# Performance work log

Measured on AMD Instinct MI355X. Metric: run time of the kernel, lower is better.

## Reference

```python
import jax, jax.numpy as jnp
import numpy as np

B, N, COUT, CIN, H, W = 16, 4, 256, 256, 64, 64


def setup_inputs() -> dict:
    key = jax.random.key(0)
    k1, k2, k3, k4 = jax.random.split(key, 4)
    x = jax.random.normal(k1, (B, CIN, H, W), jnp.float32)
    alphas = jax.random.uniform(k2, (B, N), jnp.float32)          # routing weights (lambdas)
    angles = jax.random.normal(k3, (B, N), jnp.float32) * 0.5     # thetas, mixed signs
    # kaiming_normal_(mode='fan_out', relu): std = sqrt(2 / (Cout * k * k))
    std = np.sqrt(2.0 / (COUT * 9)).astype(np.float32)
    weight = jax.random.normal(k4, (N, COUT, CIN, 3, 3), jnp.float32) * std
    return {"x": x, "alphas": alphas, "angles": angles, "weight": weight}


def _rot_mats(thetas):
    """thetas: [M] -> rotation matrices [M, 9, 9] (row, col), matching torch builder."""
    xc = jnp.cos(thetas)
    ys = jnp.sin(thetas)
    a = xc - ys
    b = xc * ys
    c = xc + ys
    z = jnp.zeros_like(xc)
    o = jnp.ones_like(xc)

    def mat(rows):
        # rows: list of 9 lists of 9 [M]-arrays -> [M, 9, 9]
        return jnp.stack([jnp.stack(r, axis=-1) for r in rows], axis=-2)

    pos = mat([
        [a, 1 - a, z, z, z, z, z, z, z],
        [z, xc - b, b, z, 1 - c + b, ys - b, z, z, z],
        [z, z, a, z, z, 1 - a, z, z, z],
        [b, ys - b, z, xc - b, 1 - c + b, z, z, z, z],
        [z, z, z, z, o, z, z, z, z],
        [z, z, z, z, 1 - c + b, xc - b, z, ys - b, b],
        [z, z, z, 1 - a, z, z, a, z, z],
        [z, z, z, ys - b, 1 - c + b, z, b, xc - b, z],
        [z, z, z, z, z, z, z, 1 - a, a],
    ])
    neg = mat([
        [c, z, z, 1 - c, z, z, z, z, z],
        [-b, xc + b, z, b - ys, 1 - a - b, z, z, z, z],
        [z, 1 - c, c, z, z, z, z, z, z],
        [z, z, z, xc + b, 1 - a - b, z, -b, b - ys, z],
        [z, z, z, z, o, z, z, z, z],
        [z, b - ys, -b, z, 1 - a - b, xc + b, z, z, z],
        [z, z, z, z, z, z, c, 1 - c, z],
        [z, z, z, z, 1 - a - b, b - ys, z, xc + b, -b],
        [z, z, z, z, z, 1 - c, z, z, c],
    ])
    m = (thetas >= 0).astype(thetas.dtype)[:, None, None]
    return m * pos + (1 - m) * neg


def reference(x, alphas, angles, weight):
    bsz, Cin, h, w = x.shape
    n, Cout = weight.shape[0], weight.shape[1]
    # [bsz, n, 9, 9] rotation matrices scaled by routing lambdas
    rm = _rot_mats(angles.reshape(-1)).reshape(bsz, n, 9, 9)
    rm = rm * alphas[:, :, None, None]
    # weights [n, Cout, Cin, 3, 3] -> [n, 9, Cout*Cin]
    Wf = weight.transpose(0, 3, 4, 1, 2).reshape(n, 9, Cout * Cin)
    # mix over kernel_number n and source tap q -> per-sample rotated kernels
    rw = jnp.einsum('bnpq,nqm->bpm', rm, Wf)          # [bsz, 9, Cout*Cin]
    rw = rw.reshape(bsz, 3, 3, Cout, Cin).transpose(0, 3, 4, 1, 2)
    rw = rw.reshape(bsz * Cout, Cin, 3, 3)
    # per-sample conv via grouped conv on flattened batch
    xr = x.reshape(1, bsz * Cin, h, w)
    out = jax.lax.conv_general_dilated(
        xr, rw, window_strides=(1, 1), padding=((1, 1), (1, 1)),
        dimension_numbers=('NCHW', 'OIHW', 'NCHW'), feature_group_count=bsz)
    return out.reshape(bsz, Cout, out.shape[2], out.shape[3])
```

## Files before the change

kernel.cpp:

```cpp
#include <hip/hip_runtime.h>
#include <hip/hip_bf16.h>

#define B_    16
#define N_    4
#define COUT  256
#define CIN   256
#define H_    64
#define W_    64
#define K_TOT (CIN * 9)
#define HW    (H_ * W_)
#define NKT   36
#define PAD   66
#define PLANE (PAD * PAD)

typedef __attribute__((ext_vector_type(8))) short short8;
typedef __attribute__((ext_vector_type(4))) float f32x4;
typedef unsigned short ushort_t;

static __device__ __forceinline__ ushort_t f2bf(float f) {
    __hip_bfloat16 h = __float2bfloat16(f);
    return *reinterpret_cast<ushort_t*>(&h);
}

typedef __attribute__((address_space(3))) unsigned int lds_u32;
typedef __attribute__((address_space(1))) const unsigned int glb_u32;
static __device__ __forceinline__ void gl_lds16(const ushort_t* g, ushort_t* l) {
    __builtin_amdgcn_global_load_lds((glb_u32*)g, (lds_u32*)l, 16, 0, 0);
}

#define BARRIER() asm volatile("s_barrier" ::: "memory")
#define VMCNTN(N) asm volatile("s_waitcnt vmcnt(" #N ")" ::: "memory")

__global__ __launch_bounds__(256)
void build_rw_kernel(const float* __restrict__ weight,
                     const float* __restrict__ alphas,
                     const float* __restrict__ angles,
                     ushort_t* __restrict__ rw) {
    __shared__ float rms[N_ * 81];
    int tid = threadIdx.x;
    int b = blockIdx.y;

    if (tid < N_) {
        int i = b * N_ + tid;
        float th = angles[i], al = alphas[i];
        float xc = cosf(th), ys = sinf(th);
        float a = xc - ys, bb = xc * ys, c = xc + ys;
        float r[81];
#pragma unroll
        for (int j = 0; j < 81; ++j) r[j] = 0.f;
        if (th >= 0.f) {
            r[0] = a;          r[1] = 1.f - a;
            r[10] = xc - bb;   r[11] = bb;       r[13] = 1.f - c + bb; r[14] = ys - bb;
            r[20] = a;         r[23] = 1.f - a;
            r[27] = bb;        r[28] = ys - bb;  r[30] = xc - bb;      r[31] = 1.f - c + bb;
            r[40] = 1.f;
            r[49] = 1.f - c + bb; r[50] = xc - bb; r[52] = ys - bb;    r[53] = bb;
            r[57] = 1.f - a;   r[60] = a;
            r[66] = ys - bb;   r[67] = 1.f - c + bb; r[69] = bb;       r[70] = xc - bb;
            r[79] = 1.f - a;   r[80] = a;
        } else {
            r[0] = c;          r[3] = 1.f - c;
            r[9] = -bb;        r[10] = xc + bb;  r[12] = bb - ys;      r[13] = 1.f - a - bb;
            r[19] = 1.f - c;   r[20] = c;
            r[30] = xc + bb;   r[31] = 1.f - a - bb; r[33] = -bb;      r[34] = bb - ys;
            r[40] = 1.f;
            r[46] = bb - ys;   r[47] = -bb;      r[49] = 1.f - a - bb; r[50] = xc + bb;
            r[60] = c;         r[61] = 1.f - c;
            r[67] = 1.f - a - bb; r[68] = bb - ys; r[70] = xc + bb;    r[71] = -bb;
            r[77] = 1.f - c;   r[80] = c;
        }
#pragma unroll
        for (int j = 0; j < 81; ++j) rms[tid * 81 + j] = r[j] * al;
    }
    __syncthreads();

    int idx = blockIdx.x * 256 + tid;
    int cout = idx >> 8, cin = idx & 255;

    float wv[N_][9];
#pragma unroll
    for (int n = 0; n < N_; ++n)
#pragma unroll
        for (int q = 0; q < 9; ++q)
            wv[n][q] = weight[(size_t)(n * (COUT * CIN) + idx) * 9 + q];

    ushort_t* dst = rw + (size_t)(b * COUT + cout) * K_TOT + cin;
#pragma unroll
    for (int p = 0; p < 9; ++p) {
        float s = 0.f;
#pragma unroll
        for (int n = 0; n < N_; ++n)
#pragma unroll
            for (int q = 0; q < 9; ++q)
                s += rms[n * 81 + p * 9 + q] * wv[n][q];
        dst[p * 256] = f2bf(s);
    }
}

__global__ __launch_bounds__(256)
void nhwc_kernel(const float* __restrict__ x, ushort_t* __restrict__ xt) {
    int y    = blockIdx.x;
    int cb32 = blockIdx.y;
    int b    = blockIdx.z;
    __shared__ ushort_t tileT[64][40];
    int t = threadIdx.x;

    ushort_t* plane = xt + (size_t)(b * 4 + (cb32 >> 1)) * PLANE * 64 + (cb32 & 1) * 32;
    const int4 z = {0, 0, 0, 0};

    int ci = t & 31, seg = t >> 5;
    const float* src = x + ((size_t)(b * CIN + cb32 * 32 + ci) * HW + y * 64 + seg * 8);
    float4 f0 = ((const float4*)src)[0];
    float4 f1 = ((const float4*)src)[1];
#pragma unroll
    for (int q = 0; q < 4; ++q) tileT[seg * 8 + q][ci]     = f2bf(((float*)&f0)[q]);
#pragma unroll
    for (int q = 0; q < 4; ++q) tileT[seg * 8 + 4 + q][ci] = f2bf(((float*)&f1)[q]);

    if (t < 8) {
        int col = (t >> 2) ? 65 : 0;
        int sg  = t & 3;
        *(int4*)(plane + ((size_t)(y + 1) * PAD + col) * 64 + sg * 8) = z;
    }
    if (y == 0) {
        for (int u = t; u < 528; u += 256) {
            int row = (u >= 264) ? 65 : 0;
            int v = (u >= 264) ? u - 264 : u;
            int px = v >> 2, sg = v & 3;
            *(int4*)(plane + ((size_t)row * PAD + px) * 64 + sg * 8) = z;
        }
    }
    __syncthreads();

    int px = t >> 2, cseg = t & 3;
    ushort_t* dst = plane + ((size_t)(y + 1) * PAD + px + 1) * 64 + cseg * 8;
    *(int4*)dst = *(const int4*)&tileT[px][cseg * 8];
}

__global__ __launch_bounds__(512, 1)
void conv_kernel(const ushort_t* __restrict__ xt,
                 const ushort_t* __restrict__ rw,
                 float* __restrict__ out) {
    int bid0 = blockIdx.x;
    int bid = (bid0 & 7) * 32 + (bid0 >> 3);
    int b     = bid >> 4;
    int ptile = bid & 15;
    int y0 = ptile * 4;
    int tid = threadIdx.x;
    int lane = tid & 63, wid = tid >> 6;
    int wm = wid >> 2, wn = wid & 3;
    int rA = lane & 15, kseg = lane >> 4;

    __shared__ __align__(16) ushort_t As[2][16384];
    __shared__ __align__(16) ushort_t Bs[2][16384];
    ushort_t* AsB = &As[0][0];
    ushort_t* BsB = &Bs[0][0];

    f32x4 acc[8][4] = {};

    const ushort_t* rwb = rw + (size_t)b * COUT * K_TOT;
    const ushort_t* xtb = xt + ((size_t)b * 4 * PLANE + (size_t)y0 * PAD) * 64;

    const int rq = tid >> 3;
    const int cs = ((tid & 7) ^ (rq & 7)) * 8;
    const int dl = tid * 8;

#define RSLOT(KH) ((((KH) << 2) | kseg) ^ (rA & 7)) * 8

#define STAGE_A2(KT, Q, Q0, Q1)                                                \
    {                                                                          \
        int p_ = (KT) >> 2, c4_ = (KT) & 3;                                    \
        int ako = p_ * 256 + c4_ * 64;                                         \
        gl_lds16(rwb + (size_t)((Q0) * 64 + rq) * K_TOT + cs + ako,            \
                 AsB + (Q) * 16384 + (Q0) * 4096 + dl);                        \
        gl_lds16(rwb + (size_t)((Q1) * 64 + rq) * K_TOT + cs + ako,            \
                 AsB + (Q) * 16384 + (Q1) * 4096 + dl);                        \
    }

#define STAGE_B2(KT, Q, Q0, Q1)                                                \
    {                                                                          \
        int p_ = (KT) >> 2, c4_ = (KT) & 3;                                    \
        int ph_ = p_ / 3, pw_ = p_ - 3 * ph_;                                  \
        const ushort_t* sb_ = xtb + (size_t)(c4_ * PLANE + ph_ * PAD + pw_) * 64; \
        gl_lds16(sb_ + (size_t)((Q0) * PAD + rq) * 64 + cs,                    \
                 BsB + (Q) * 16384 + (Q0) * 4096 + dl);                        \
        gl_lds16(sb_ + (size_t)((Q1) * PAD + rq) * 64 + cs,                    \
                 BsB + (Q) * 16384 + (Q1) * 4096 + dl);                        \
    }

#define READ_AF(Q, MH, KH)                                                     \
    _Pragma("unroll")                                                          \
    for (int mi = 0; mi < 4; ++mi) {                                           \
        int row = wm * 128 + (MH) * 64 + mi * 16 + rA;                         \
        af[mi] = *(const short8*)(AsB + (Q) * 16384 + row * 64 + RSLOT(KH));   \
    }

#define READ_BF(Q, KH)                                                         \
    _Pragma("unroll")                                                          \
    for (int ni = 0; ni < 4; ++ni) {                                           \
        int row = wn * 64 + ni * 16 + rA;                                      \
        bf[ni] = *(const short8*)(BsB + (Q) * 16384 + row * 64 + RSLOT(KH));   \
    }

#define DO_MFMA(MH)                                                            \
    __builtin_amdgcn_s_setprio(1);                                             \
    _Pragma("unroll")                                                          \
    for (int mi = 0; mi < 4; ++mi)                                             \
        _Pragma("unroll")                                                      \
        for (int ni = 0; ni < 4; ++ni)                                         \
            acc[(MH) * 4 + mi][ni] = __builtin_amdgcn_mfma_f32_16x16x32_bf16(  \
                af[mi], bf[ni], acc[(MH) * 4 + mi][ni], 0, 0, 0);              \
    __builtin_amdgcn_s_setprio(0);

    STAGE_B2(0, 0, 0, 1);
    STAGE_B2(0, 0, 2, 3);
    STAGE_A2(0, 0, 0, 2);
    STAGE_A2(0, 0, 1, 3);
    VMCNTN(2);
    BARRIER();

    short8 af[4], bf[4];
    for (int kt = 0; kt < NKT; ++kt) {
        int q = kt & 1, qn = q ^ 1;
        bool more = (kt + 1 < NKT);
        READ_AF(q, 0, 0);
        READ_BF(q, 0);
        if (more) STAGE_B2(kt + 1, qn, 0, 1);
        BARRIER();
        DO_MFMA(0);
        if (more) { VMCNTN(2); } else { VMCNTN(0); }
        BARRIER();
        READ_AF(q, 1, 0);
        if (more) STAGE_B2(kt + 1, qn, 2, 3);
        BARRIER();
        DO_MFMA(1);
        BARRIER();
        READ_AF(q, 0, 1);
        READ_BF(q, 1);
        if (more) STAGE_A2(kt + 1, qn, 0, 2);
        BARRIER();
        DO_MFMA(0);
        BARRIER();
        READ_AF(q, 1, 1);
        if (more) STAGE_A2(kt + 1, qn, 1, 3);
        BARRIER();
        DO_MFMA(1);
        VMCNTN(2);
        BARRIER();
    }
#undef STAGE_A2
#undef STAGE_B2
#undef READ_AF
#undef READ_BF
#undef DO_MFMA
#undef RSLOT

    int row0 = (lane >> 4) * 4;
    int col  = lane & 15;
    float* outb = out + (size_t)b * COUT * HW + ptile * 256;
#pragma unroll
    for (int am = 0; am < 8; ++am)
#pragma unroll
        for (int an = 0; an < 4; ++an)
#pragma unroll
            for (int rr = 0; rr < 4; ++rr) {
                int m = wm * 128 + am * 16 + row0 + rr;
                int n = wn * 64 + an * 16 + col;
                outb[(size_t)m * HW + n] = acc[am][an][rr];
            }
}

extern "C" void kernel_launch(void* const* d_in, const int* in_sizes, int n_in,
                              void* d_out, int out_size, void* d_ws, size_t ws_size,
                              hipStream_t stream) {
    const float* x      = (const float*)d_in[0];
    const float* alphas = (const float*)d_in[1];
    const float* angles = (const float*)d_in[2];
    const float* weight = (const float*)d_in[3];
    float* out = (float*)d_out;

    ushort_t* rw = (ushort_t*)d_ws;
    ushort_t* xt = (ushort_t*)((char*)d_ws + (size_t)B_ * COUT * K_TOT * 2);

    build_rw_kernel<<<dim3(COUT * CIN / 256, B_), 256, 0, stream>>>(weight, alphas, angles, rw);
    nhwc_kernel<<<dim3(64, 8, B_), 256, 0, stream>>>(x, xt);
    conv_kernel<<<256, 512, 0, stream>>>(xt, rw, out);
}
```

Measured before the change: 107.5 us.

## Triple-buffer the activation tile to prefetch two K-steps ahead

The B (activation) LDS buffer grows from two stages to three, so B tiles are loaded two iterations ahead while A weights stay double-buffered one step ahead. The staging order inside each iteration is reshuffled so A loads are issued first and B loads later, and the vmcnt waits are retuned to allow more outstanding global-to-LDS loads. The aim is to hide more global-load latency behind the MFMA work. The cost is 32 KB more LDS (160 KB total), which leaves less headroom and makes the wait-count bookkeeping more fragile.

```diff
diff --git a/kernel.cpp b/kernel.cpp
--- a/kernel.cpp
+++ b/kernel.cpp
@@ -152,7 +152,7 @@
     int rA = lane & 15, kseg = lane >> 4;
 
     __shared__ __align__(16) ushort_t As[2][16384];
-    __shared__ __align__(16) ushort_t Bs[2][16384];
+    __shared__ __align__(16) ushort_t Bs[3][16384];
     ushort_t* AsB = &As[0][0];
     ushort_t* BsB = &Bs[0][0];
 
@@ -167,39 +167,39 @@
 
 #define RSLOT(KH) ((((KH) << 2) | kseg) ^ (rA & 7)) * 8
 
-#define STAGE_A2(KT, Q, Q0, Q1)                                                \
+#define STAGE_A2(KT, BUFO, Q0, Q1)                                             \
     {                                                                          \
         int p_ = (KT) >> 2, c4_ = (KT) & 3;                                    \
         int ako = p_ * 256 + c4_ * 64;                                         \
         gl_lds16(rwb + (size_t)((Q0) * 64 + rq) * K_TOT + cs + ako,            \
-                 AsB + (Q) * 16384 + (Q0) * 4096 + dl);                        \
+                 AsB + (BUFO) + (Q0) * 4096 + dl);                             \
         gl_lds16(rwb + (size_t)((Q1) * 64 + rq) * K_TOT + cs + ako,            \
-                 AsB + (Q) * 16384 + (Q1) * 4096 + dl);                        \
-    }
-
-#define STAGE_B2(KT, Q, Q0, Q1)                                                \
+                 AsB + (BUFO) + (Q1) * 4096 + dl);                             \
+    }
+
+#define STAGE_B2(KT, BUFO, Q0, Q1)                                             \
     {                                                                          \
         int p_ = (KT) >> 2, c4_ = (KT) & 3;                                    \
         int ph_ = p_ / 3, pw_ = p_ - 3 * ph_;                                  \
         const ushort_t* sb_ = xtb + (size_t)(c4_ * PLANE + ph_ * PAD + pw_) * 64; \
         gl_lds16(sb_ + (size_t)((Q0) * PAD + rq) * 64 + cs,                    \
-                 BsB + (Q) * 16384 + (Q0) * 4096 + dl);                        \
+                 BsB + (BUFO) + (Q0) * 4096 + dl);                             \
         gl_lds16(sb_ + (size_t)((Q1) * PAD + rq) * 64 + cs,                    \
-                 BsB + (Q) * 16384 + (Q1) * 4096 + dl);                        \
-    }
-
-#define READ_AF(Q, MH, KH)                                                     \
+                 BsB + (BUFO) + (Q1) * 4096 + dl);                             \
+    }
+
+#define READ_AF(BUFO, MH, KH)                                                  \
     _Pragma("unroll")                                                          \
     for (int mi = 0; mi < 4; ++mi) {                                           \
         int row = wm * 128 + (MH) * 64 + mi * 16 + rA;                         \
-        af[mi] = *(const short8*)(AsB + (Q) * 16384 + row * 64 + RSLOT(KH));   \
-    }
-
-#define READ_BF(Q, KH)                                                         \
+        af[mi] = *(const short8*)(AsB + (BUFO) + row * 64 + RSLOT(KH));        \
+    }
+
+#define READ_BF(BUFO, KH)                                                      \
     _Pragma("unroll")                                                          \
     for (int ni = 0; ni < 4; ++ni) {                                           \
         int row = wn * 64 + ni * 16 + rA;                                      \
-        bf[ni] = *(const short8*)(BsB + (Q) * 16384 + row * 64 + RSLOT(KH));   \
+        bf[ni] = *(const short8*)(BsB + (BUFO) + row * 64 + RSLOT(KH));        \
     }
 
 #define DO_MFMA(MH)                                                            \
@@ -216,37 +216,48 @@
     STAGE_B2(0, 0, 2, 3);
     STAGE_A2(0, 0, 0, 2);
     STAGE_A2(0, 0, 1, 3);
-    VMCNTN(2);
+    STAGE_B2(1, 16384, 0, 1);
+    STAGE_B2(1, 16384, 2, 3);
+    VMCNTN(6);
     BARRIER();
 
     short8 af[4], bf[4];
+    int bq = 0;
     for (int kt = 0; kt < NKT; ++kt) {
-        int q = kt & 1, qn = q ^ 1;
-        bool more = (kt + 1 < NKT);
-        READ_AF(q, 0, 0);
-        READ_BF(q, 0);
-        if (more) STAGE_B2(kt + 1, qn, 0, 1);
+        int bsq = bq + 2; if (bsq >= 3) bsq -= 3;
+        const int abuf  = (kt & 1) << 14;
+        const int anbuf = ((kt + 1) & 1) << 14;
+        const int bbuf  = bq * 16384;
+        const int bsbuf = bsq * 16384;
+        bool moreA = (kt + 1 < NKT), moreB = (kt + 2 < NKT);
+
+        READ_AF(abuf, 0, 0);
+        READ_BF(bbuf, 0);
+        if (moreA) STAGE_A2(kt + 1, anbuf, 0, 2);
         BARRIER();
         DO_MFMA(0);
-        if (more) { VMCNTN(2); } else { VMCNTN(0); }
-        BARRIER();
-        READ_AF(q, 1, 0);
-        if (more) STAGE_B2(kt + 1, qn, 2, 3);
+        if (moreA) { VMCNTN(6); } else { VMCNTN(0); }
+        BARRIER();
+        READ_AF(abuf, 1, 0);
+        if (moreA) STAGE_A2(kt + 1, anbuf, 1, 3);
         BARRIER();
         DO_MFMA(1);
         BARRIER();
-        READ_AF(q, 0, 1);
-        READ_BF(q, 1);
-        if (more) STAGE_A2(kt + 1, qn, 0, 2);
+        READ_AF(abuf, 0, 1);
+        READ_BF(bbuf, 1);
+        if (moreB) STAGE_B2(kt + 2, bsbuf, 0, 1);
         BARRIER();
         DO_MFMA(0);
         BARRIER();
-        READ_AF(q, 1, 1);
-        if (more) STAGE_A2(kt + 1, qn, 1, 3);
+        READ_AF(abuf, 1, 1);
+        if (moreB) STAGE_B2(kt + 2, bsbuf, 2, 3);
         BARRIER();
         DO_MFMA(1);
-        VMCNTN(2);
-        BARRIER();
+        if (moreB)      { VMCNTN(6); }
+        else if (moreA) { VMCNTN(2); }
+        else            { VMCNTN(0); }
+        BARRIER();
+        bq = (bq == 2) ? 0 : bq + 1;
     }
 #undef STAGE_A2
 #undef STAGE_B2
```

After: 107.2 us. Within noise of the previous version (-0.2%).

## Switch conv GEMM to 32x32x16 MFMA tiles with two-phase K pipeline

Applied to the files above, without the earlier changes.

Replaces the 16x16x32 bf16 MFMA tiling with 32x32x16 MFMAs, so each wave holds a 4x2 grid of 32x32 accumulators. The LDS fragment reads, the swizzled slot addressing and the output scatter are rewritten to match the new layout. The per-k-tile schedule shrinks from four barrier phases to two, staging half of the next tile's A and B loads in each phase. The aim is fewer LDS reads per MFMA and fewer barriers, at the cost of more register pressure from the larger fragment arrays.

```diff
diff --git a/kernel.cpp b/kernel.cpp
--- a/kernel.cpp
+++ b/kernel.cpp
@@ -14,7 +14,7 @@
 #define PLANE (PAD * PAD)
 
 typedef __attribute__((ext_vector_type(8))) short short8;
-typedef __attribute__((ext_vector_type(4))) float f32x4;
+typedef __attribute__((ext_vector_type(16))) float f32x16;
 typedef unsigned short ushort_t;
 
 static __device__ __forceinline__ ushort_t f2bf(float f) {
@@ -149,14 +149,15 @@
     int tid = threadIdx.x;
     int lane = tid & 63, wid = tid >> 6;
     int wm = wid >> 2, wn = wid & 3;
-    int rA = lane & 15, kseg = lane >> 4;
+    int rA = lane & 31;
+    int hi = lane >> 5;
 
     __shared__ __align__(16) ushort_t As[2][16384];
     __shared__ __align__(16) ushort_t Bs[2][16384];
     ushort_t* AsB = &As[0][0];
     ushort_t* BsB = &Bs[0][0];
 
-    f32x4 acc[8][4] = {};
+    f32x16 acc[4][2] = {};
 
     const ushort_t* rwb = rw + (size_t)b * COUT * K_TOT;
     const ushort_t* xtb = xt + ((size_t)b * 4 * PLANE + (size_t)y0 * PAD) * 64;
@@ -165,108 +166,104 @@
     const int cs = ((tid & 7) ^ (rq & 7)) * 8;
     const int dl = tid * 8;
 
-#define RSLOT(KH) ((((KH) << 2) | kseg) ^ (rA & 7)) * 8
-
-#define STAGE_A2(KT, Q, Q0, Q1)                                                \
+#define RSLOT(KS) ((((KS) * 2 + hi) ^ (lane & 7)) * 8)
+
+#define STAGE_A1(KT, BUFO, QTR)                                                \
     {                                                                          \
         int p_ = (KT) >> 2, c4_ = (KT) & 3;                                    \
         int ako = p_ * 256 + c4_ * 64;                                         \
-        gl_lds16(rwb + (size_t)((Q0) * 64 + rq) * K_TOT + cs + ako,            \
-                 AsB + (Q) * 16384 + (Q0) * 4096 + dl);                        \
-        gl_lds16(rwb + (size_t)((Q1) * 64 + rq) * K_TOT + cs + ako,            \
-                 AsB + (Q) * 16384 + (Q1) * 4096 + dl);                        \
-    }
-
-#define STAGE_B2(KT, Q, Q0, Q1)                                                \
+        gl_lds16(rwb + (size_t)((QTR) * 64 + rq) * K_TOT + cs + ako,           \
+                 AsB + (BUFO) + (QTR) * 4096 + dl);                            \
+    }
+
+#define STAGE_B1(KT, BUFO, QTR)                                                \
     {                                                                          \
         int p_ = (KT) >> 2, c4_ = (KT) & 3;                                    \
         int ph_ = p_ / 3, pw_ = p_ - 3 * ph_;                                  \
         const ushort_t* sb_ = xtb + (size_t)(c4_ * PLANE + ph_ * PAD + pw_) * 64; \
-        gl_lds16(sb_ + (size_t)((Q0) * PAD + rq) * 64 + cs,                    \
-                 BsB + (Q) * 16384 + (Q0) * 4096 + dl);                        \
-        gl_lds16(sb_ + (size_t)((Q1) * PAD + rq) * 64 + cs,                    \
-                 BsB + (Q) * 16384 + (Q1) * 4096 + dl);                        \
-    }
-
-#define READ_AF(Q, MH, KH)                                                     \
+        gl_lds16(sb_ + (size_t)((QTR) * PAD + rq) * 64 + cs,                   \
+                 BsB + (BUFO) + (QTR) * 4096 + dl);                            \
+    }
+
+#define READ_AF(BUFO, MH)                                                      \
     _Pragma("unroll")                                                          \
-    for (int mi = 0; mi < 4; ++mi) {                                           \
-        int row = wm * 128 + (MH) * 64 + mi * 16 + rA;                         \
-        af[mi] = *(const short8*)(AsB + (Q) * 16384 + row * 64 + RSLOT(KH));   \
-    }
-
-#define READ_BF(Q, KH)                                                         \
+    for (int mi = 0; mi < 2; ++mi) {                                           \
+        int row = wm * 128 + ((MH) * 2 + mi) * 32 + rA;                        \
+        _Pragma("unroll")                                                      \
+        for (int ks = 0; ks < 4; ++ks)                                         \
+            af[mi][ks] = *(const short8*)(AsB + (BUFO) + row * 64 + RSLOT(ks));\
+    }
+
+#define READ_BF(BUFO)                                                          \
     _Pragma("unroll")                                                          \
-    for (int ni = 0; ni < 4; ++ni) {                                           \
-        int row = wn * 64 + ni * 16 + rA;                                      \
-        bf[ni] = *(const short8*)(BsB + (Q) * 16384 + row * 64 + RSLOT(KH));   \
+    for (int ni = 0; ni < 2; ++ni) {                                           \
+        int row = wn * 64 + ni * 32 + rA;                                      \
+        _Pragma("unroll")                                                      \
+        for (int ks = 0; ks < 4; ++ks)                                         \
+            bf[ni][ks] = *(const short8*)(BsB + (BUFO) + row * 64 + RSLOT(ks));\
     }
 
 #define DO_MFMA(MH)                                                            \
     __builtin_amdgcn_s_setprio(1);                                             \
     _Pragma("unroll")                                                          \
-    for (int mi = 0; mi < 4; ++mi)                                             \
+    for (int mi = 0; mi < 2; ++mi)                                             \
         _Pragma("unroll")                                                      \
-        for (int ni = 0; ni < 4; ++ni)                                         \
-            acc[(MH) * 4 + mi][ni] = __builtin_amdgcn_mfma_f32_16x16x32_bf16(  \
-                af[mi], bf[ni], acc[(MH) * 4 + mi][ni], 0, 0, 0);              \
+        for (int ni = 0; ni < 2; ++ni)                                         \
+            _Pragma("unroll")                                                  \
+            for (int ks = 0; ks < 4; ++ks)                                     \
+                acc[(MH) * 2 + mi][ni] = __builtin_amdgcn_mfma_f32_32x32x16_bf16( \
+                    af[mi][ks], bf[ni][ks], acc[(MH) * 2 + mi][ni], 0, 0, 0);  \
     __builtin_amdgcn_s_setprio(0);
 
-    STAGE_B2(0, 0, 0, 1);
-    STAGE_B2(0, 0, 2, 3);
-    STAGE_A2(0, 0, 0, 2);
-    STAGE_A2(0, 0, 1, 3);
+    STAGE_A1(0, 0, 0); STAGE_A1(0, 0, 2);
+    STAGE_B1(0, 0, 0); STAGE_B1(0, 0, 1);
+    STAGE_B1(0, 0, 2); STAGE_B1(0, 0, 3);
+    STAGE_A1(0, 0, 1); STAGE_A1(0, 0, 3);
     VMCNTN(2);
     BARRIER();
 
-    short8 af[4], bf[4];
+    short8 af[2][4], bf[2][4];
     for (int kt = 0; kt < NKT; ++kt) {
-        int q = kt & 1, qn = q ^ 1;
+        const int qb  = (kt & 1) << 14;
+        const int qnb = ((kt + 1) & 1) << 14;
         bool more = (kt + 1 < NKT);
-        READ_AF(q, 0, 0);
-        READ_BF(q, 0);
-        if (more) STAGE_B2(kt + 1, qn, 0, 1);
+        READ_BF(qb);
+        READ_AF(qb, 0);
+        if (more) {
+            STAGE_A1(kt + 1, qnb, 0); STAGE_A1(kt + 1, qnb, 2);
+            STAGE_B1(kt + 1, qnb, 0); STAGE_B1(kt + 1, qnb, 1);
+        }
         BARRIER();
         DO_MFMA(0);
+        if (more) { VMCNTN(4); } else { VMCNTN(0); }
+        BARRIER();
+        READ_AF(qb, 1);
+        if (more) {
+            STAGE_B1(kt + 1, qnb, 2); STAGE_B1(kt + 1, qnb, 3);
+            STAGE_A1(kt + 1, qnb, 1); STAGE_A1(kt + 1, qnb, 3);
+        }
+        BARRIER();
+        DO_MFMA(1);
         if (more) { VMCNTN(2); } else { VMCNTN(0); }
         BARRIER();
-        READ_AF(q, 1, 0);
-        if (more) STAGE_B2(kt + 1, qn, 2, 3);
-        BARRIER();
-        DO_MFMA(1);
-        BARRIER();
-        READ_AF(q, 0, 1);
-        READ_BF(q, 1);
-        if (more) STAGE_A2(kt + 1, qn, 0, 2);
-        BARRIER();
-        DO_MFMA(0);
-        BARRIER();
-        READ_AF(q, 1, 1);
-        if (more) STAGE_A2(kt + 1, qn, 1, 3);
-        BARRIER();
-        DO_MFMA(1);
-        VMCNTN(2);
-        BARRIER();
-    }
-#undef STAGE_A2
-#undef STAGE_B2
+    }
+#undef STAGE_A1
+#undef STAGE_B1
 #undef READ_AF
 #undef READ_BF
 #undef DO_MFMA
 #undef RSLOT
 
-    int row0 = (lane >> 4) * 4;
-    int col  = lane & 15;
     float* outb = out + (size_t)b * COUT * HW + ptile * 256;
 #pragma unroll
-    for (int am = 0; am < 8; ++am)
-#pragma unroll
-        for (int an = 0; an < 4; ++an)
-#pragma unroll
-            for (int rr = 0; rr < 4; ++rr) {
-                int m = wm * 128 + am * 16 + row0 + rr;
-                int n = wn * 64 + an * 16 + col;
-                outb[(size_t)m * HW + n] = acc[am][an][rr];
+    for (int mt = 0; mt < 4; ++mt)
+#pragma unroll
+        for (int nt = 0; nt < 2; ++nt)
+#pragma unroll
+            for (int r = 0; r < 16; ++r) {
+                int m = wm * 128 + mt * 32 + (r & 3) + 8 * (r >> 2) + 4 * hi;
+                int n = wn * 64 + nt * 32 + rA;
+                outb[(size_t)m * HW + n] = acc[mt][nt][r];
             }
 }
 
```

New measurement: 116.2 us. +8.2%, slower.
